# Kernel tuning notes

Measured on AMD Instinct MI355X. Metric: run time of the kernel, lower is better.

Reference implementation:

```python
import jax, jax.numpy as jnp
import numpy as np
from jax import lax

N_NODES = 100000
N_EDGES = 1600000
UNITS = 64
DEPTH_EMB = 12
DEPTH_PAR = 5
EPS = 1e-5


def setup_inputs() -> dict:
    key = jax.random.key(0)
    ks = jax.random.split(key, 24)
    x = jax.random.normal(ks[0], (N_NODES, 1), dtype=jnp.float32)
    edge_index = jax.random.randint(ks[1], (2, N_EDGES), 0, N_NODES, dtype=jnp.int32)
    s = 1.0 / np.sqrt(UNITS)
    # GCN conv params: first layer maps feats=1 -> 64, remaining 11 map 64 -> 64
    conv_w0 = jax.random.normal(ks[2], (1, UNITS), dtype=jnp.float32)
    conv_w = jax.random.normal(ks[3], (DEPTH_EMB - 1, UNITS, UNITS), dtype=jnp.float32) * s
    conv_b = jnp.zeros((DEPTH_EMB, UNITS), dtype=jnp.float32)
    # GraphNorm params (applied after every conv except the last)
    gn_gamma = jnp.ones((DEPTH_EMB - 1, UNITS), dtype=jnp.float32)
    gn_beta = jnp.zeros((DEPTH_EMB - 1, UNITS), dtype=jnp.float32)
    gn_alpha = jnp.ones((DEPTH_EMB - 1, UNITS), dtype=jnp.float32)
    # ParNet heads: 4 residual 64->64 linears + final 64->1
    phe_w = jax.random.normal(ks[4], (DEPTH_PAR - 1, UNITS, UNITS), dtype=jnp.float32) * s
    phe_b = jnp.zeros((DEPTH_PAR - 1, UNITS), dtype=jnp.float32)
    phe_wl = jax.random.normal(ks[5], (UNITS, 1), dtype=jnp.float32) * s
    phe_bl = jnp.zeros((1,), dtype=jnp.float32)
    heu_w = jax.random.normal(ks[6], (DEPTH_PAR - 1, UNITS, UNITS), dtype=jnp.float32) * s
    heu_b = jnp.zeros((DEPTH_PAR - 1, UNITS), dtype=jnp.float32)
    heu_wl = jax.random.normal(ks[7], (UNITS, 1), dtype=jnp.float32) * s
    heu_bl = jnp.zeros((1,), dtype=jnp.float32)
    return {"x": x, "edge_index": edge_index,
            "conv_w0": conv_w0, "conv_w": conv_w, "conv_b": conv_b,
            "gn_gamma": gn_gamma, "gn_beta": gn_beta, "gn_alpha": gn_alpha,
            "phe_w": phe_w, "phe_b": phe_b, "phe_wl": phe_wl, "phe_bl": phe_bl,
            "heu_w": heu_w, "heu_b": heu_b, "heu_wl": heu_wl, "heu_bl": heu_bl}


def _graph_norm(h, gamma, beta, alpha):
    # single-graph GraphNorm: per-feature mean over nodes, mean-scale alpha
    mean = jnp.mean(h, axis=0, keepdims=True)            # [1, C]
    hc = h - alpha * mean
    var = jnp.mean(hc * hc, axis=0, keepdims=True)       # [1, C]
    return gamma * hc * lax.rsqrt(var + EPS) + beta


def _parnet(h, ws, bs, wl, bl):
    for i in range(DEPTH_PAR - 1):
        h = jax.nn.relu(h + h @ ws[i] + bs[i])
    return jax.nn.sigmoid(h @ wl + bl)[:, 0]             # [N]


def reference(x, edge_index, conv_w0, conv_w, conv_b, gn_gamma, gn_beta, gn_alpha,
              phe_w, phe_b, phe_wl, phe_bl, heu_w, heu_b, heu_wl, heu_bl):
    n = x.shape[0]
    src, dst = edge_index[0], edge_index[1]
    # GCN symmetric normalization with self-loops
    deg = 1.0 + jax.ops.segment_sum(jnp.ones_like(src, dtype=x.dtype), dst, num_segments=n)
    dinv = lax.rsqrt(deg)                                # [N]
    norm_e = (dinv[src] * dinv[dst])[:, None]            # [E, 1]
    self_norm = (dinv * dinv)[:, None]                   # [N, 1]

    h = x
    for i in range(DEPTH_EMB):
        w = conv_w0 if i == 0 else conv_w[i - 1]
        h = h @ w                                        # [N, 64]
        agg = jax.ops.segment_sum(h[src] * norm_e, dst, num_segments=n)
        h = agg + h * self_norm + conv_b[i]
        if i < DEPTH_EMB - 1:
            h = _graph_norm(h, gn_gamma[i], gn_beta[i], gn_alpha[i])
            h = jax.nn.silu(h)

    phe = _parnet(h, phe_w, phe_b, phe_wl, phe_bl)
    heu = _parnet(h, heu_w, heu_b, heu_wl, heu_bl)
    return (phe, heu)
```

## Files before the change

### kernel.cpp

```cpp
#include <hip/hip_runtime.h>
#include <hip/hip_bf16.h>
#include <hip/hip_fp16.h>
#include <math.h>

#define UNITS 64
#define DEPTH_EMB 12
#define DEPTH_PAR 5
#define GN_EPS 1e-5f


__global__ void k_deg(const int* __restrict__ dst, int* __restrict__ cnt, int E) {
    int e = blockIdx.x * blockDim.x + threadIdx.x;
    if (e < E) atomicAdd(&cnt[dst[e]], 1);
}

__global__ void k_dinv(const int* __restrict__ cnt, float* __restrict__ dinv, int n) {
    int i = blockIdx.x * blockDim.x + threadIdx.x;
    if (i < n) dinv[i] = rsqrtf(1.0f + (float)cnt[i]);
}

__global__ void k_chunksum(const int* __restrict__ cnt, int* __restrict__ csum, int n) {
    __shared__ int sd[256];
    int base = blockIdx.x * 1024;
    int s = 0;
    for (int i = threadIdx.x; i < 1024; i += 256) {
        int idx = base + i;
        if (idx < n) s += cnt[idx];
    }
    sd[threadIdx.x] = s;
    __syncthreads();
    for (int off = 128; off > 0; off >>= 1) {
        if (threadIdx.x < off) sd[threadIdx.x] += sd[threadIdx.x + off];
        __syncthreads();
    }
    if (threadIdx.x == 0) csum[blockIdx.x] = sd[0];
}

__global__ void k_scansum(const int* __restrict__ csum, int* __restrict__ coff,
                          int* __restrict__ rowptr, int nchunks) {
    __shared__ int sd[256];
    int tid = threadIdx.x;
    int v = (tid < nchunks) ? csum[tid] : 0;
    sd[tid] = v;
    __syncthreads();
    for (int off = 1; off < 256; off <<= 1) {
        int t = (tid >= off) ? sd[tid - off] : 0;
        __syncthreads();
        sd[tid] += t;
        __syncthreads();
    }
    if (tid < nchunks) coff[tid] = sd[tid] - v;
    if (tid == 0) rowptr[0] = 0;
}

__global__ void k_scanfinal(const int* __restrict__ cnt, const int* __restrict__ coff,
                            int* __restrict__ rowptr, int n) {
    __shared__ int sd[1024];
    int base = blockIdx.x * 1024;
    int tid = threadIdx.x;
    int idx = base + tid;
    int v = (idx < n) ? cnt[idx] : 0;
    sd[tid] = v;
    __syncthreads();
    for (int off = 1; off < 1024; off <<= 1) {
        int t = (tid >= off) ? sd[tid - off] : 0;
        __syncthreads();
        sd[tid] += t;
        __syncthreads();
    }
    if (idx < n) rowptr[idx + 1] = coff[blockIdx.x] + sd[tid];
}

__global__ void k_fill(const int* __restrict__ src, const int* __restrict__ dst,
                       const int* __restrict__ rowptr, int* __restrict__ fill,
                       int* __restrict__ srcs, int E) {
    int e = blockIdx.x * blockDim.x + threadIdx.x;
    if (e >= E) return;
    int s = src[e], d = dst[e];
    int p = rowptr[d] + atomicAdd(&fill[d], 1);
    srcs[p] = s;
}


__global__ void k_l0(const float* __restrict__ x, const float* __restrict__ w0,
                     const float* __restrict__ dinv, __half* __restrict__ h2, int n) {
    int gid = blockIdx.x * blockDim.x + threadIdx.x;
    if (gid >= n * UNITS) return;
    int node = gid >> 6, c = gid & 63;
    h2[gid] = __float2half(x[node] * w0[c] * dinv[node]);
}


template <int DO_STATS>
__global__ void k_gather(const __half* __restrict__ h2, float* __restrict__ h,
                         const int* __restrict__ rowptr, const int* __restrict__ srcs,
                         const float* __restrict__ dinv, const float* __restrict__ b,
                         float* __restrict__ stats, int n) {
    int lane = threadIdx.x & 63;
    int wib = threadIdx.x >> 6;
    int wpb = blockDim.x >> 6;
    int gwave = blockIdx.x * wpb + wib;
    int nwaves = gridDim.x * wpb;
    float bj = b[lane];
    float s1 = 0.0f, s2 = 0.0f;

    for (int nd = gwave; nd < n; nd += nwaves) {
        int node = __builtin_amdgcn_readfirstlane(nd);
        int beg = rowptr[node], end = rowptr[node + 1];
        float di = dinv[node];
        float acc0 = __half2float(h2[(size_t)node * UNITS + lane]);
        float acc1 = 0.0f, acc2 = 0.0f, acc3 = 0.0f;
        int j = beg;
        for (; j + 8 <= end; j += 8) {
            int i0 = srcs[j + 0], i1 = srcs[j + 1], i2 = srcs[j + 2], i3 = srcs[j + 3];
            int i4 = srcs[j + 4], i5 = srcs[j + 5], i6 = srcs[j + 6], i7 = srcs[j + 7];
            float v0 = __half2float(h2[(size_t)i0 * UNITS + lane]);
            float v1 = __half2float(h2[(size_t)i1 * UNITS + lane]);
            float v2 = __half2float(h2[(size_t)i2 * UNITS + lane]);
            float v3 = __half2float(h2[(size_t)i3 * UNITS + lane]);
            float v4 = __half2float(h2[(size_t)i4 * UNITS + lane]);
            float v5 = __half2float(h2[(size_t)i5 * UNITS + lane]);
            float v6 = __half2float(h2[(size_t)i6 * UNITS + lane]);
            float v7 = __half2float(h2[(size_t)i7 * UNITS + lane]);
            acc0 += v0; acc1 += v1; acc2 += v2; acc3 += v3;
            acc0 += v4; acc1 += v5; acc2 += v6; acc3 += v7;
        }
        for (; j + 4 <= end; j += 4) {
            int i0 = srcs[j + 0], i1 = srcs[j + 1], i2 = srcs[j + 2], i3 = srcs[j + 3];
            float v0 = __half2float(h2[(size_t)i0 * UNITS + lane]);
            float v1 = __half2float(h2[(size_t)i1 * UNITS + lane]);
            float v2 = __half2float(h2[(size_t)i2 * UNITS + lane]);
            float v3 = __half2float(h2[(size_t)i3 * UNITS + lane]);
            acc0 += v0; acc1 += v1; acc2 += v2; acc3 += v3;
        }
        for (; j < end; ++j) acc0 += __half2float(h2[(size_t)srcs[j] * UNITS + lane]);
        float acc = (acc0 + acc1) + (acc2 + acc3);
        float hv = fmaf(acc, di, bj);
        h[(size_t)node * UNITS + lane] = hv;
        if (DO_STATS) {
            s1 += hv;
            s2 = fmaf(hv, hv, s2);
        }
    }

    if (DO_STATS) {
        __shared__ float sd[2][4][UNITS];
        sd[0][wib][lane] = s1;
        sd[1][wib][lane] = s2;
        __syncthreads();
        if (threadIdx.x < UNITS) {
            float a1 = 0.0f, a2 = 0.0f;
            for (int r = 0; r < wpb; ++r) {
                a1 += sd[0][r][lane];
                a2 += sd[1][r][lane];
            }
            atomicAdd(&stats[lane], a1);
            atomicAdd(&stats[UNITS + lane], a2);
        }
    }
}


__global__ void k_nsl(const float* __restrict__ in, __half* __restrict__ out,
                      const float* __restrict__ W, const float* __restrict__ dinv,
                      const float* __restrict__ stats, const float* __restrict__ gamma,
                      const float* __restrict__ beta, const float* __restrict__ alpha,
                      float inv_n, int n) {
    __shared__ float lds[4][UNITS];
    int lane = threadIdx.x & 63;
    int wib = threadIdx.x >> 6;
    int wpb = blockDim.x >> 6;
    int gwave = blockIdx.x * wpb + wib;
    int nwaves = gridDim.x * wpb;

    float w[UNITS];
#pragma unroll
    for (int k = 0; k < UNITS; ++k) w[k] = W[k * UNITS + lane];

    float m = stats[lane] * inv_n;
    float ex2 = stats[UNITS + lane] * inv_n;
    float al = alpha[lane];
    float var = ex2 - m * m * (2.0f * al - al * al);
    float g = gamma[lane] * rsqrtf(var + GN_EPS);
    float A = g;
    float B = beta[lane] - g * al * m;

    for (int nd = gwave; nd < n; nd += nwaves) {
        int node = __builtin_amdgcn_readfirstlane(nd);
        float hv = in[(size_t)node * UNITS + lane];
        float t = fmaf(hv, A, B);
        t = t / (1.0f + __expf(-t));
        lds[wib][lane] = t;
        float di = dinv[node];
        float a0 = 0.0f, a1 = 0.0f, a2 = 0.0f, a3 = 0.0f;
#pragma unroll
        for (int k = 0; k < UNITS; k += 4) {
            float4 tv = *(const float4*)&lds[wib][k];
            a0 = fmaf(tv.x, w[k + 0], a0);
            a1 = fmaf(tv.y, w[k + 1], a1);
            a2 = fmaf(tv.z, w[k + 2], a2);
            a3 = fmaf(tv.w, w[k + 3], a3);
        }
        float acc = (a0 + a1) + (a2 + a3);
        out[(size_t)node * UNITS + lane] = __float2half(acc * di);
    }
}


__global__ void k_linear_par(const float* __restrict__ in, float* __restrict__ out,
                             const float* __restrict__ W, const float* __restrict__ b, int n) {
    int lane = threadIdx.x & 63;
    int wib = threadIdx.x >> 6;
    int wpb = blockDim.x >> 6;
    int gwave = blockIdx.x * wpb + wib;
    int nwaves = gridDim.x * wpb;

    float w[UNITS];
#pragma unroll
    for (int k = 0; k < UNITS; ++k) w[k] = W[k * UNITS + lane];
    float bj = b[lane];

    for (int nd = gwave; nd < n; nd += nwaves) {
        int node = __builtin_amdgcn_readfirstlane(nd);
        const float* __restrict__ row = in + (size_t)node * UNITS;
        float a0 = 0.0f, a1 = 0.0f, a2 = 0.0f, a3 = 0.0f;
#pragma unroll
        for (int k = 0; k < UNITS; k += 4) {
            a0 = fmaf(row[k + 0], w[k + 0], a0);
            a1 = fmaf(row[k + 1], w[k + 1], a1);
            a2 = fmaf(row[k + 2], w[k + 2], a2);
            a3 = fmaf(row[k + 3], w[k + 3], a3);
        }
        float acc = (a0 + a1) + (a2 + a3) + row[lane] + bj;
        acc = fmaxf(acc, 0.0f);
        out[(size_t)node * UNITS + lane] = acc;
    }
}


__global__ void k_linear_head(const float* __restrict__ in, const float* __restrict__ W,
                              const float* __restrict__ b, const float* __restrict__ wl,
                              const float* __restrict__ bl, float* __restrict__ out, int n) {
    int lane = threadIdx.x & 63;
    int wib = threadIdx.x >> 6;
    int wpb = blockDim.x >> 6;
    int gwave = blockIdx.x * wpb + wib;
    int nwaves = gridDim.x * wpb;

    float w[UNITS];
#pragma unroll
    for (int k = 0; k < UNITS; ++k) w[k] = W[k * UNITS + lane];
    float bj = b[lane];
    float wv = wl[lane];
    float blv = bl[0];

    for (int nd = gwave; nd < n; nd += nwaves) {
        int node = __builtin_amdgcn_readfirstlane(nd);
        const float* __restrict__ row = in + (size_t)node * UNITS;
        float a0 = 0.0f, a1 = 0.0f, a2 = 0.0f, a3 = 0.0f;
#pragma unroll
        for (int k = 0; k < UNITS; k += 4) {
            a0 = fmaf(row[k + 0], w[k + 0], a0);
            a1 = fmaf(row[k + 1], w[k + 1], a1);
            a2 = fmaf(row[k + 2], w[k + 2], a2);
            a3 = fmaf(row[k + 3], w[k + 3], a3);
        }
        float acc = (a0 + a1) + (a2 + a3) + row[lane] + bj;
        acc = fmaxf(acc, 0.0f);
        float p = acc * wv;
#pragma unroll
        for (int off = 32; off > 0; off >>= 1) p += __shfl_xor(p, off, 64);
        if (lane == 0) out[node] = 1.0f / (1.0f + __expf(-(p + blv)));
    }
}


extern "C" void kernel_launch(void* const* d_in, const int* in_sizes, int n_in,
                              void* d_out, int out_size, void* d_ws, size_t ws_size,
                              hipStream_t stream) {
    const float* x = (const float*)d_in[0];
    const int* ei = (const int*)d_in[1];
    const float* conv_w0 = (const float*)d_in[2];
    const float* conv_w = (const float*)d_in[3];
    const float* conv_b = (const float*)d_in[4];
    const float* gn_gamma = (const float*)d_in[5];
    const float* gn_beta = (const float*)d_in[6];
    const float* gn_alpha = (const float*)d_in[7];
    const float* phe_w = (const float*)d_in[8];
    const float* phe_b = (const float*)d_in[9];
    const float* phe_wl = (const float*)d_in[10];
    const float* phe_bl = (const float*)d_in[11];
    const float* heu_w = (const float*)d_in[12];
    const float* heu_b = (const float*)d_in[13];
    const float* heu_wl = (const float*)d_in[14];
    const float* heu_bl = (const float*)d_in[15];

    const int N = in_sizes[0];
    const int E = in_sizes[1] / 2;
    const int NC = N * UNITS;
    const int NCHUNK1024 = (N + 1023) / 1024;

    const int* src = ei;
    const int* dstp = ei + E;

    char* w = (char*)d_ws;
    float* dinv = (float*)w;  w += (size_t)N * 4;
    float* h = (float*)w;     w += (size_t)NC * 4;
    float* hx = (float*)w;    w += (size_t)NC * 4;
    float* h3 = (float*)w;    w += (size_t)NC * 4;
    float* stats = (float*)w; w += (size_t)DEPTH_EMB * 128 * 4;
    int* cnt = (int*)w;       w += (size_t)N * 4;
    int* rowptr = (int*)w;    w += (size_t)(N + 1) * 4;
    int* fillc = (int*)w;     w += (size_t)N * 4;
    int* srcs = (int*)w;      w += (size_t)(E + 16) * 4;
    int* csum = (int*)w;      w += 256 * 4;
    int* coff = (int*)w;      w += 256 * 4;

    __half* h2 = (__half*)hx;
    float* out = (float*)d_out;

    const int B = 256;
    const int gE = (E + B - 1) / B;
    const int gN = (N + B - 1) / B;
    const int gNC = (NC + B - 1) / B;

    hipMemsetAsync(cnt, 0, (size_t)N * 4, stream);
    hipMemsetAsync(fillc, 0, (size_t)N * 4, stream);
    hipMemsetAsync(stats, 0, (size_t)DEPTH_EMB * 128 * 4, stream);
    k_deg<<<gE, B, 0, stream>>>(dstp, cnt, E);
    k_dinv<<<gN, B, 0, stream>>>(cnt, dinv, N);
    k_chunksum<<<NCHUNK1024, 256, 0, stream>>>(cnt, csum, N);
    k_scansum<<<1, 256, 0, stream>>>(csum, coff, rowptr, NCHUNK1024);
    k_scanfinal<<<NCHUNK1024, 1024, 0, stream>>>(cnt, coff, rowptr, N);
    k_fill<<<gE, B, 0, stream>>>(src, dstp, rowptr, fillc, srcs, E);

    k_l0<<<gNC, B, 0, stream>>>(x, conv_w0, dinv, h2, N);
    for (int i = 0; i < DEPTH_EMB; ++i) {
        float* st = stats + (size_t)i * 128;
        if (i < DEPTH_EMB - 1) {
            k_gather<1><<<2048, B, 0, stream>>>(h2, h, rowptr, srcs, dinv,
                                                conv_b + (size_t)i * UNITS, st, N);
            k_nsl<<<2048, B, 0, stream>>>(h, h2, conv_w + (size_t)i * UNITS * UNITS,
                                          dinv, st,
                                          gn_gamma + (size_t)i * UNITS,
                                          gn_beta + (size_t)i * UNITS,
                                          gn_alpha + (size_t)i * UNITS,
                                          1.0f / (float)N, N);
        } else {
            k_gather<0><<<2048, B, 0, stream>>>(h2, h, rowptr, srcs, dinv,
                                                conv_b + (size_t)i * UNITS, st, N);
        }
    }

    for (int head = 0; head < 2; ++head) {
        const float* wsrc = head == 0 ? phe_w : heu_w;
        const float* bsrc = head == 0 ? phe_b : heu_b;
        const float* wl = head == 0 ? phe_wl : heu_wl;
        const float* bl = head == 0 ? phe_bl : heu_bl;
        float* o = out + (size_t)head * N;

        k_linear_par<<<2048, B, 0, stream>>>(h, h3, wsrc, bsrc, N);
        k_linear_par<<<2048, B, 0, stream>>>(h3, hx, wsrc + (size_t)1 * UNITS * UNITS,
                                             bsrc + (size_t)1 * UNITS, N);
        k_linear_par<<<2048, B, 0, stream>>>(hx, h3, wsrc + (size_t)2 * UNITS * UNITS,
                                             bsrc + (size_t)2 * UNITS, N);
        k_linear_head<<<2048, B, 0, stream>>>(h3, wsrc + (size_t)3 * UNITS * UNITS,
                                              bsrc + (size_t)3 * UNITS, wl, bl, o, N);
    }
}
```

Measured before the change: 1.553 ms.

## Bucket edges by destination block before CSR fill to localize srcs writes

Replaces the single-pass atomic CSR fill with a two-level counting sort: per-block histograms of destination buckets (256 nodes each), a scan of those histograms, a scatter of (dst,src) pairs into bucket order, then a fill pass over the bucketed pairs. The intent is that the final atomic fill and srcs writes become spatially local, so the random scattered writes and atomics cost less. It adds four extra kernel launches and an extra 8-byte-per-edge pass through a reused workspace buffer, and the resulting order within each CSR row still depends on atomics.

```diff
diff --git a/kernel.cpp b/kernel.cpp
--- a/kernel.cpp
+++ b/kernel.cpp
@@ -7,6 +7,8 @@
 #define DEPTH_EMB 12
 #define DEPTH_PAR 5
 #define GN_EPS 1e-5f
+#define NFILLB 256
+#define MAXNB 512
 
 
 __global__ void k_deg(const int* __restrict__ dst, int* __restrict__ cnt, int E) {
@@ -71,14 +73,81 @@
     if (idx < n) rowptr[idx + 1] = coff[blockIdx.x] + sd[tid];
 }
 
-__global__ void k_fill(const int* __restrict__ src, const int* __restrict__ dst,
-                       const int* __restrict__ rowptr, int* __restrict__ fill,
-                       int* __restrict__ srcs, int E) {
-    int e = blockIdx.x * blockDim.x + threadIdx.x;
-    if (e >= E) return;
-    int s = src[e], d = dst[e];
-    int p = rowptr[d] + atomicAdd(&fill[d], 1);
-    srcs[p] = s;
+
+__global__ void k_bcount(const int* __restrict__ dst, int* __restrict__ table,
+                         int E, int nb, int epb) {
+    __shared__ int hist[MAXNB];
+    int tid = threadIdx.x;
+    for (int i = tid; i < nb; i += 256) hist[i] = 0;
+    __syncthreads();
+    int e0 = blockIdx.x * epb;
+    int e1 = min(e0 + epb, E);
+    for (int e = e0 + tid; e < e1; e += 256) atomicAdd(&hist[dst[e] >> 8], 1);
+    __syncthreads();
+    for (int i = tid; i < nb; i += 256) table[i * NFILLB + blockIdx.x] = hist[i];
+}
+
+__global__ void k_bscan(int* __restrict__ table, int* __restrict__ btot) {
+    __shared__ int sd[NFILLB];
+    int b = blockIdx.x;
+    int tid = threadIdx.x;
+    int v = table[b * NFILLB + tid];
+    sd[tid] = v;
+    __syncthreads();
+    for (int off = 1; off < NFILLB; off <<= 1) {
+        int t = (tid >= off) ? sd[tid - off] : 0;
+        __syncthreads();
+        sd[tid] += t;
+        __syncthreads();
+    }
+    table[b * NFILLB + tid] = sd[tid] - v;
+    if (tid == NFILLB - 1) btot[b] = sd[NFILLB - 1];
+}
+
+__global__ void k_boffscan(const int* __restrict__ btot, int* __restrict__ boff, int nb) {
+    __shared__ int sd[MAXNB];
+    int tid = threadIdx.x;
+    int v = (tid < nb) ? btot[tid] : 0;
+    sd[tid] = v;
+    __syncthreads();
+    for (int off = 1; off < MAXNB; off <<= 1) {
+        int t = (tid >= off) ? sd[tid - off] : 0;
+        __syncthreads();
+        sd[tid] += t;
+        __syncthreads();
+    }
+    if (tid < nb) boff[tid] = sd[tid] - v;
+}
+
+__global__ void k_bscatter(const int* __restrict__ src, const int* __restrict__ dst,
+                           const int* __restrict__ table, const int* __restrict__ boff,
+                           unsigned long long* __restrict__ pairs, int E, int nb, int epb) {
+    __shared__ int hist[MAXNB];
+    int tid = threadIdx.x;
+    for (int i = tid; i < nb; i += 256) hist[i] = 0;
+    __syncthreads();
+    int e0 = blockIdx.x * epb;
+    int e1 = min(e0 + epb, E);
+    for (int e = e0 + tid; e < e1; e += 256) {
+        int d = dst[e];
+        int b = d >> 8;
+        int local = atomicAdd(&hist[b], 1);
+        int p = boff[b] + table[b * NFILLB + blockIdx.x] + local;
+        pairs[p] = ((unsigned long long)(unsigned)d << 32) | (unsigned)src[e];
+    }
+}
+
+__global__ void k_pfill(const unsigned long long* __restrict__ pairs,
+                        const int* __restrict__ rowptr, int* __restrict__ fillc,
+                        int* __restrict__ srcs, int E) {
+    int stride = gridDim.x * blockDim.x;
+    for (int idx = blockIdx.x * blockDim.x + threadIdx.x; idx < E; idx += stride) {
+        unsigned long long pr = pairs[idx];
+        int s = (int)(pr & 0xffffffffu);
+        int d = (int)(pr >> 32);
+        int p = rowptr[d] + atomicAdd(&fillc[d], 1);
+        srcs[p] = s;
+    }
 }
 
 
@@ -299,6 +368,8 @@
     const int E = in_sizes[1] / 2;
     const int NC = N * UNITS;
     const int NCHUNK1024 = (N + 1023) / 1024;
+    const int NB = (N + 255) / 256;
+    const int EPB = (E + NFILLB - 1) / NFILLB;
 
     const int* src = ei;
     const int* dstp = ei + E;
@@ -315,8 +386,12 @@
     int* srcs = (int*)w;      w += (size_t)(E + 16) * 4;
     int* csum = (int*)w;      w += 256 * 4;
     int* coff = (int*)w;      w += 256 * 4;
+    int* table = (int*)w;     w += (size_t)MAXNB * NFILLB * 4;
+    int* btot = (int*)w;      w += MAXNB * 4;
+    int* boff = (int*)w;      w += MAXNB * 4;
 
     __half* h2 = (__half*)hx;
+    unsigned long long* pairs = (unsigned long long*)h3;
     float* out = (float*)d_out;
 
     const int B = 256;
@@ -332,7 +407,11 @@
     k_chunksum<<<NCHUNK1024, 256, 0, stream>>>(cnt, csum, N);
     k_scansum<<<1, 256, 0, stream>>>(csum, coff, rowptr, NCHUNK1024);
     k_scanfinal<<<NCHUNK1024, 1024, 0, stream>>>(cnt, coff, rowptr, N);
-    k_fill<<<gE, B, 0, stream>>>(src, dstp, rowptr, fillc, srcs, E);
+    k_bcount<<<NFILLB, 256, 0, stream>>>(dstp, table, E, NB, EPB);
+    k_bscan<<<NB, NFILLB, 0, stream>>>(table, btot);
+    k_boffscan<<<1, MAXNB, 0, stream>>>(btot, boff, NB);
+    k_bscatter<<<NFILLB, 256, 0, stream>>>(src, dstp, table, boff, pairs, E, NB, EPB);
+    k_pfill<<<2048, B, 0, stream>>>(pairs, rowptr, fillc, srcs, E);
 
     k_l0<<<gNC, B, 0, stream>>>(x, conv_w0, dinv, h2, N);
     for (int i = 0; i < DEPTH_EMB; ++i) {
```

New measurement: 1.534 ms, median of 2. About the same (-1.2%).
